# Performance work log

Hardware: AMD Instinct MI355X
Metric: run time of the kernel (lower is better)

The kernel has to match this reference:

```python
import jax, jax.numpy as jnp
import numpy as np

N, E = 50000, 800000
IN, HID, OUT, H = 128, 64, 64, 2
NC, EC = 5, 2  # node / edge num classes
NUM_ITER, GAMMA = 2, 1.0


def gat_conv(x, src, dst, eattr, W, att_s, att_d, We, att_e, b, n_nodes):
    """PyG GATConv with concat=False, edge_dim, add_self_loops(fill='mean')."""
    Hh, C = att_s.shape
    # self loops; loop edge_attr = per-dst-node mean of incident edge features
    ones_e = jnp.ones((src.shape[0],), x.dtype)
    deg = jax.ops.segment_sum(ones_e, dst, num_segments=n_nodes)
    loop_attr = jax.ops.segment_sum(eattr, dst, num_segments=n_nodes) / jnp.maximum(deg, 1.0)[:, None]
    loop = jnp.arange(n_nodes)
    src = jnp.concatenate([src, loop])
    dst = jnp.concatenate([dst, loop])
    eattr = jnp.concatenate([eattr, loop_attr], axis=0)
    h = (x @ W).reshape(n_nodes, Hh, C)            # [N,H,C]
    e = (eattr @ We).reshape(-1, Hh, C)            # [E',H,C]
    a_s = jnp.einsum('nhc,hc->nh', h, att_s)
    a_d = jnp.einsum('nhc,hc->nh', h, att_d)
    a_e = jnp.einsum('ehc,hc->eh', e, att_e)
    a = jax.nn.leaky_relu(a_s[src] + a_d[dst] + a_e, 0.2)  # [E',H]
    amax = jax.ops.segment_max(a, dst, num_segments=n_nodes)
    ea = jnp.exp(a - amax[dst])
    denom = jax.ops.segment_sum(ea, dst, num_segments=n_nodes)
    alpha = ea / (denom[dst] + 1e-16)
    out = jax.ops.segment_sum(alpha[:, :, None] * h[src], dst, num_segments=n_nodes)
    return out.mean(axis=1) + b                     # concat=False -> head mean


def factor_graph(node_logits, edge_logits, src, dst, node_fw, edge_fw):
    n = node_logits.shape[0]
    p_n = jax.nn.softmax(node_logits, axis=-1)
    p_e = jax.nn.softmax(edge_logits, axis=-1)
    ones_e = jnp.ones((src.shape[0],), node_logits.dtype)
    deg = jax.ops.segment_sum(ones_e, src, num_segments=n) + jax.ops.segment_sum(ones_e, dst, num_segments=n)
    avg_ef = edge_fw[1:, 1:].mean()
    avg_nf = node_fw[1:, 1:].mean()
    for _ in range(NUM_ITER):
        nab = 1.0 - p_n[:, 0]
        ena = jnp.maximum(nab[src], nab[dst])                       # [E]
        new_ab = p_e[:, 1:] * (1.0 + GAMMA * ena[:, None] * avg_ef)
        p_e = jnp.concatenate([p_e[:, :1], new_ab], axis=-1)
        p_e = p_e / p_e.sum(axis=-1, keepdims=True)
        eab = 1.0 - p_e[:, 0]
        s = jax.ops.segment_sum(eab, src, num_segments=n) + jax.ops.segment_sum(eab, dst, num_segments=n)
        mean = s / (deg + 1e-6)
        new_nab = p_n[:, 1:] * (1.0 + GAMMA * mean[:, None] * avg_nf)
        p_n = jnp.concatenate([p_n[:, :1], new_nab], axis=-1)
        p_n = p_n / p_n.sum(axis=-1, keepdims=True)
    return jnp.log(p_n + 1e-9), jnp.log(p_e + 1e-9)


def setup_inputs() -> dict:
    key = jax.random.key(0)
    ks = jax.random.split(key, 24)
    s = 0.1
    d = dict(
        x=jax.random.normal(ks[0], (N, IN), jnp.float32),
        edge_index=jax.random.randint(ks[1], (2, E), 0, N),
        edge_attr=jax.random.normal(ks[2], (E, 2), jnp.float32),
        W1=jax.random.normal(ks[3], (IN, H * HID), jnp.float32) * s,
        att_src1=jax.random.normal(ks[4], (H, HID), jnp.float32) * s,
        att_dst1=jax.random.normal(ks[5], (H, HID), jnp.float32) * s,
        We1=jax.random.normal(ks[6], (2, H * HID), jnp.float32) * s,
        att_e1=jax.random.normal(ks[7], (H, HID), jnp.float32) * s,
        b1=jnp.zeros((HID,), jnp.float32),
        W2=jax.random.normal(ks[8], (HID, H * OUT), jnp.float32) * s,
        att_src2=jax.random.normal(ks[9], (H, OUT), jnp.float32) * s,
        att_dst2=jax.random.normal(ks[10], (H, OUT), jnp.float32) * s,
        We2=jax.random.normal(ks[11], (2, H * OUT), jnp.float32) * s,
        att_e2=jax.random.normal(ks[12], (H, OUT), jnp.float32) * s,
        b2=jnp.zeros((OUT,), jnp.float32),
        Wn=jax.random.normal(ks[13], (OUT, NC), jnp.float32) * s,
        bn=jnp.zeros((NC,), jnp.float32),
        Wec=jax.random.normal(ks[14], (OUT, EC), jnp.float32) * s,
        bec=jnp.zeros((EC,), jnp.float32),
        node_fw=jnp.ones((NC, EC), jnp.float32),
        edge_fw=jnp.ones((EC, NC), jnp.float32),
    )
    return d


def reference(x, edge_index, edge_attr, W1, att_src1, att_dst1, We1, att_e1, b1,
              W2, att_src2, att_dst2, We2, att_e2, b2, Wn, bn, Wec, bec,
              node_fw, edge_fw):
    src, dst = edge_index[0], edge_index[1]
    h = gat_conv(x, src, dst, edge_attr, W1, att_src1, att_dst1, We1, att_e1, b1, N)
    h = jax.nn.relu(h)
    h = gat_conv(h, src, dst, edge_attr, W2, att_src2, att_dst2, We2, att_e2, b2, N)
    node_logits = h @ Wn + bn                       # [N,NC]
    edge_emb = (h[src] + h[dst]) * 0.5              # [E,OUT]
    edge_logits = edge_emb @ Wec + bec              # [E,EC]
    return factor_graph(node_logits, edge_logits, src, dst, node_fw, edge_fw)
```

## Files before the change

### kernel.cpp

```cpp
#include <hip/hip_runtime.h>
#include <math.h>


static inline int cdiv_i(long long a, long long b) { return (int)((a + b - 1) / b); }

#define BSH 8
#define CBK 8

typedef __attribute__((ext_vector_type(8))) short bf16x8s;
typedef __attribute__((ext_vector_type(4))) float f32x4;

__device__ __forceinline__ float fexp(float x) {
  return __builtin_amdgcn_exp2f(x * 1.44269504088896f);
}
__device__ __forceinline__ float flog(float x) {
  return __builtin_amdgcn_logf(x) * 0.693147180559945f;
}
__device__ __forceinline__ float frcp(float x) {
  return __builtin_amdgcn_rcpf(x);
}

__device__ __forceinline__ unsigned short bf16r(float x) {
  unsigned u = __float_as_uint(x);
  return (unsigned short)((u + 0x7fffu + ((u >> 16) & 1u)) >> 16);
}
__device__ __forceinline__ unsigned pack_bf2(float a, float b) {
  unsigned ua = __float_as_uint(a), ub = __float_as_uint(b);
  unsigned ra = (ua + 0x7fffu + ((ua >> 16) & 1u)) >> 16;
  unsigned rb = (ub + 0x7fffu + ((ub >> 16) & 1u)) & 0xffff0000u;
  return ra | rb;
}
__device__ __forceinline__ float bf_lo(unsigned v) { return __uint_as_float(v << 16); }
__device__ __forceinline__ float bf_hi(unsigned v) { return __uint_as_float(v & 0xffff0000u); }

__global__ __launch_bounds__(256)
void k_prep(const float* __restrict__ W1, const float* __restrict__ as1,
            const float* __restrict__ ad1, const float* __restrict__ atte1,
            const float* __restrict__ We1,
            const float* __restrict__ W2, const float* __restrict__ as2,
            const float* __restrict__ ad2, const float* __restrict__ atte2,
            const float* __restrict__ We2,
            const float* __restrict__ node_fw, const float* __restrict__ edge_fw,
            const float* __restrict__ bec, float* __restrict__ consts,
            unsigned short* __restrict__ wf1, unsigned short* __restrict__ wf2,
            int* __restrict__ cur_d, int* __restrict__ cur_s) {
  __shared__ float wext1[128 * 4], wext2[64 * 4];
  int t = threadIdx.x;
  cur_d[t] = 0; cur_s[t] = 0;
  if (t == 0) {
    for (int h = 0; h < 2; ++h)
      for (int k = 0; k < 2; ++k) {
        float s1 = 0.f, s2 = 0.f;
        for (int c = 0; c < 64; ++c) {
          s1 += We1[k * 128 + h * 64 + c] * atte1[h * 64 + c];
          s2 += We2[k * 128 + h * 64 + c] * atte2[h * 64 + c];
        }
        consts[h * 2 + k] = s1;
        consts[4 + h * 2 + k] = s2;
      }
    float ef = 0.f;
    for (int j = 1; j < 5; ++j) ef += edge_fw[5 + j];
    consts[8] = ef * 0.25f;
    float nf = 0.f;
    for (int i = 1; i < 5; ++i) nf += node_fw[i * 2 + 1];
    consts[9] = nf * 0.25f;
    consts[10] = bec[1] - bec[0];
  }
  for (int o = t; o < 128 * 4; o += 256) {
    int k = o >> 2, j = o & 3;
    const float* att = (j < 2 ? as1 : ad1) + (j & 1) * 64;
    const float* wr = W1 + k * 128 + (j & 1) * 64;
    float s = 0.f;
    for (int c = 0; c < 64; ++c) s += wr[c] * att[c];
    wext1[o] = s;
  }
  for (int o = t; o < 64 * 4; o += 256) {
    int k = o >> 2, j = o & 3;
    const float* att = (j < 2 ? as2 : ad2) + (j & 1) * 64;
    const float* wr = W2 + k * 128 + (j & 1) * 64;
    float s = 0.f;
    for (int c = 0; c < 64; ++c) s += wr[c] * att[c];
    wext2[o] = s;
  }
  __syncthreads();
  for (int o = t; o < 4 * 9 * 512; o += 256) {
    int kc = o / (9 * 512), rem = o % (9 * 512);
    int ct = rem / 512, li = rem % 512;
    int lane = li >> 3, j = li & 7;
    int k = kc * 32 + ((lane >> 4) << 3) + j, c = lane & 15;
    float v = (ct < 8) ? W1[k * 128 + ct * 16 + c] : (c < 4 ? wext1[k * 4 + c] : 0.f);
    wf1[o] = bf16r(v);
  }
  for (int o = t; o < 2 * 9 * 512; o += 256) {
    int kc = o / (9 * 512), rem = o % (9 * 512);
    int ct = rem / 512, li = rem % 512;
    int lane = li >> 3, j = li & 7;
    int k = kc * 32 + ((lane >> 4) << 3) + j, c = lane & 15;
    float v = (ct < 8) ? W2[k * 128 + ct * 16 + c] : (c < 4 ? wext2[k * 4 + c] : 0.f);
    wf2[o] = bf16r(v);
  }
}

__global__ void k_bkt_hist(const int* __restrict__ src, const int* __restrict__ dst,
                           int* __restrict__ hist_d, int* __restrict__ hist_s,
                           int nbkt, int E) {
  __shared__ int hd[256], hs[256];
  int t = threadIdx.x;
  hd[t] = 0; hs[t] = 0;
  __syncthreads();
  for (int e = blockIdx.x * blockDim.x + t; e < E; e += gridDim.x * blockDim.x) {
    atomicAdd(&hd[dst[e] >> BSH], 1);
    atomicAdd(&hs[src[e] >> BSH], 1);
  }
  __syncthreads();
  if (t < nbkt) {
    if (hd[t]) atomicAdd(&hist_d[t], hd[t]);
    if (hs[t]) atomicAdd(&hist_s[t], hs[t]);
  }
}

__global__ void k_bkt_scan(int* __restrict__ cur_d, int* __restrict__ base_d,
                           int* __restrict__ cur_s, int* __restrict__ base_s, int nbkt) {
  __shared__ int l[256];
  int t = threadIdx.x;
  int v = (t < nbkt) ? cur_d[t] : 0;
  l[t] = v; __syncthreads();
  for (int off = 1; off < 256; off <<= 1) {
    int x = (t >= off) ? l[t - off] : 0; __syncthreads();
    l[t] += x; __syncthreads();
  }
  int incl = l[t];
  if (t < nbkt) { base_d[t] = incl - v; cur_d[t] = incl - v; }
  if (t == nbkt - 1) base_d[nbkt] = incl;
  __syncthreads();
  v = (t < nbkt) ? cur_s[t] : 0;
  l[t] = v; __syncthreads();
  for (int off = 1; off < 256; off <<= 1) {
    int x = (t >= off) ? l[t - off] : 0; __syncthreads();
    l[t] += x; __syncthreads();
  }
  incl = l[t];
  if (t < nbkt) { base_s[t] = incl - v; cur_s[t] = incl - v; }
  if (t == nbkt - 1) base_s[nbkt] = incl;
}

__global__ __launch_bounds__(256)
void k_bkt_scatter(const int* __restrict__ src, const int* __restrict__ dst,
                   const float* __restrict__ eattr2,
                   int* __restrict__ cur_d, int* __restrict__ cur_s,
                   int4* __restrict__ stage_d, int2* __restrict__ stage_s,
                   int nbkt, int E) {
  __shared__ int cd[256], cs[256], bd[256], bs[256];
  int t = threadIdx.x;
  cd[t] = 0; cs[t] = 0;
  __syncthreads();
  int base = blockIdx.x * 256 * CBK;
  int s[CBK], d[CBK]; unsigned ep[CBK];
#pragma unroll
  for (int c = 0; c < CBK; ++c) {
    int e = base + c * 256 + t;
    if (e < E) {
      s[c] = src[e]; d[c] = dst[e];
      float2 ev = *(const float2*)&eattr2[2 * e];
      ep[c] = pack_bf2(ev.x, ev.y);
      atomicAdd(&cd[d[c] >> BSH], 1);
      atomicAdd(&cs[s[c] >> BSH], 1);
    } else s[c] = -1;
  }
  __syncthreads();
  if (t < nbkt) {
    bd[t] = cd[t] ? atomicAdd(&cur_d[t], cd[t]) : 0;
    bs[t] = cs[t] ? atomicAdd(&cur_s[t], cs[t]) : 0;
    cd[t] = 0; cs[t] = 0;
  }
  __syncthreads();
#pragma unroll
  for (int c = 0; c < CBK; ++c) {
    if (s[c] < 0) continue;
    int db = d[c] >> BSH, sb = s[c] >> BSH;
    int pos = bd[db] + atomicAdd(&cd[db], 1);
    stage_d[pos] = make_int4(s[c], d[c], (int)ep[c], 0);
    int pos2 = bs[sb] + atomicAdd(&cs[sb], 1);
    stage_s[pos2] = make_int2(s[c], d[c]);
  }
}

__global__ __launch_bounds__(256)
void k_bkt_sort(const int4* __restrict__ stage_d, const int* __restrict__ base_d,
                int* __restrict__ rowptr_d, int2* __restrict__ rec,
                const int2* __restrict__ stage_s, const int* __restrict__ base_s,
                int* __restrict__ rowptr_s, int* __restrict__ srcnbr,
                int N, int nbkt) {
  int t = threadIdx.x;
  __shared__ int cnt[256], cur[256], l[256];
  if ((int)blockIdx.x < nbkt) {
    int b = blockIdx.x;
    int nlo = b << BSH;
    int b0 = base_d[b], b1 = base_d[b + 1];
    cnt[t] = 0;
    __syncthreads();
    for (int j = b0 + t; j < b1; j += 256)
      atomicAdd(&cnt[stage_d[j].y - nlo], 1);
    __syncthreads();
    int v = cnt[t];
    l[t] = v; __syncthreads();
    for (int off = 1; off < 256; off <<= 1) {
      int x = (t >= off) ? l[t - off] : 0; __syncthreads();
      l[t] += x; __syncthreads();
    }
    int excl = l[t] - v;
    if (nlo + t < N) rowptr_d[nlo + t] = b0 + excl;
    cur[t] = excl;
    __syncthreads();
    for (int j = b0 + t; j < b1; j += 256) {
      int4 r = stage_d[j];
      int pos = b0 + atomicAdd(&cur[r.y - nlo], 1);
      rec[pos] = make_int2(r.x, r.z);
    }
  } else {
    int b = blockIdx.x - nbkt;
    int nlo = b << BSH;
    int b0 = base_s[b], b1 = base_s[b + 1];
    cnt[t] = 0;
    __syncthreads();
    for (int j = b0 + t; j < b1; j += 256)
      atomicAdd(&cnt[stage_s[j].x - nlo], 1);
    __syncthreads();
    int v = cnt[t];
    l[t] = v; __syncthreads();
    for (int off = 1; off < 256; off <<= 1) {
      int x = (t >= off) ? l[t - off] : 0; __syncthreads();
      l[t] += x; __syncthreads();
    }
    int excl = l[t] - v;
    if (nlo + t < N) rowptr_s[nlo + t] = b0 + excl;
    cur[t] = excl;
    __syncthreads();
    for (int j = b0 + t; j < b1; j += 256) {
      int2 r = stage_s[j];
      int pos = b0 + atomicAdd(&cur[r.x - nlo], 1);
      srcnbr[pos] = r.y;
    }
  }
}

template<int K>
__global__ __launch_bounds__(256)
void k_gemm_att_mfma(const float* __restrict__ A, const unsigned short* __restrict__ Wf,
                     unsigned* __restrict__ h16, float* __restrict__ asd, int N) {
  int wv = threadIdx.x >> 6, lane = threadIdx.x & 63;
  int r0 = blockIdx.x * 64 + wv * 16;
  int arow = r0 + (lane & 15);
  int kbase = (lane >> 4) * 8;
  f32x4 acc[9];
#pragma unroll
  for (int ct = 0; ct < 9; ++ct) acc[ct] = (f32x4){0.f, 0.f, 0.f, 0.f};

#pragma unroll
  for (int kc = 0; kc < K; kc += 32) {
    float4 v0 = make_float4(0.f, 0.f, 0.f, 0.f);
    float4 v1 = make_float4(0.f, 0.f, 0.f, 0.f);
    if (arow < N) {
      const float* ap = A + (long long)arow * K + kc + kbase;
      v0 = *(const float4*)ap;
      v1 = *(const float4*)(ap + 4);
    }
    bf16x8s a;
    a[0] = (short)bf16r(v0.x); a[1] = (short)bf16r(v0.y);
    a[2] = (short)bf16r(v0.z); a[3] = (short)bf16r(v0.w);
    a[4] = (short)bf16r(v1.x); a[5] = (short)bf16r(v1.y);
    a[6] = (short)bf16r(v1.z); a[7] = (short)bf16r(v1.w);
    const unsigned short* wp = Wf + (size_t)(kc >> 5) * 9 * 512 + lane * 8;
#pragma unroll
    for (int ct = 0; ct < 9; ++ct) {
      bf16x8s b = *(const bf16x8s*)(wp + ct * 512);
      acc[ct] = __builtin_amdgcn_mfma_f32_16x16x32_bf16(a, b, acc[ct], 0, 0, 0);
    }
  }
  int c = lane & 15;
  int orow = r0 + (lane >> 4) * 4;
#pragma unroll
  for (int r = 0; r < 4; ++r) {
    int gr = orow + r;
    if (gr >= N) continue;
#pragma unroll
    for (int ct = 0; ct < 4; ++ct)
      h16[((long long)gr << 6) | (ct * 16 + c)] = pack_bf2(acc[ct][r], acc[ct + 4][r]);
    if (c < 4) asd[gr * 4 + c] = acc[8][r];
  }
}

template<bool RELU, bool HEAD>
__global__ __launch_bounds__(256)
void k_gat_pull(const int* __restrict__ rowptr, const int2* __restrict__ rec,
                const float* __restrict__ asd, const unsigned* __restrict__ h16,
                const float* __restrict__ we, const float* __restrict__ bias,
                const float* __restrict__ Wn, const float* __restrict__ bn,
                const float* __restrict__ Wec,
                float* __restrict__ out, float* __restrict__ p_n,
                int2* __restrict__ fgn8, int N, int E) {
  __shared__ int2 ed[4][64];
  int wv = threadIdx.x >> 6, lane = threadIdx.x & 63;
  int g = lane >> 4;
  int tl = lane & 15;
  int d = blockIdx.x * 16 + wv * 4 + g;
  if (d >= N) return;
  int r0 = rowptr[d];
  int r1 = (d + 1 < N) ? rowptr[d + 1] : E;
  int deg = r1 - r0;
  float4 Ad = *(const float4*)&asd[4 * d];
  float w0 = we[0], w1 = we[1], w2 = we[2], w3 = we[3];
  float den0 = 0.f, den1 = 0.f, se0 = 0.f, se1 = 0.f;
  float accA[4] = {0.f, 0.f, 0.f, 0.f}, accB[4] = {0.f, 0.f, 0.f, 0.f};
  int2* edg = &ed[wv][g << 4];
  for (int cb = 0; cb < deg; cb += 16) {
    int j = cb + tl;
    int s = 0; unsigned eapk = 0;
    if (j < deg) {
      int2 rc = rec[r0 + j];
      s = rc.x;
      unsigned ep = (unsigned)rc.y;
      float e0 = bf_lo(ep), e1 = bf_hi(ep);
      float4 As = *(const float4*)&asd[4 * s];
      float x0 = As.x + Ad.z + e0 * w0 + e1 * w1;
      float x1 = As.y + Ad.w + e0 * w2 + e1 * w3;
      x0 = x0 >= 0.f ? x0 : 0.2f * x0;
      x1 = x1 >= 0.f ? x1 : 0.2f * x1;
      float ea0 = fexp(x0), ea1 = fexp(x1);
      eapk = pack_bf2(ea0, ea1);
      den0 += ea0; den1 += ea1; se0 += e0; se1 += e1;
    }
    edg[tl] = make_int2(s, (int)eapk);
    int m = min(16, deg - cb);
    int j2 = 0;
    for (; j2 + 2 <= m; j2 += 2) {
      int2 va = edg[j2];
      int2 vb = edg[j2 + 1];
      uint4 qa = *(const uint4*)&h16[((long long)va.x << 6) | (tl << 2)];
      uint4 qb = *(const uint4*)&h16[((long long)vb.x << 6) | (tl << 2)];
      float a0 = bf_lo((unsigned)va.y), a1 = bf_hi((unsigned)va.y);
      float b0 = bf_lo((unsigned)vb.y), b1 = bf_hi((unsigned)vb.y);
      accA[0] += a0 * bf_lo(qa.x); accB[0] += a1 * bf_hi(qa.x);
      accA[1] += a0 * bf_lo(qa.y); accB[1] += a1 * bf_hi(qa.y);
      accA[2] += a0 * bf_lo(qa.z); accB[2] += a1 * bf_hi(qa.z);
      accA[3] += a0 * bf_lo(qa.w); accB[3] += a1 * bf_hi(qa.w);
      accA[0] += b0 * bf_lo(qb.x); accB[0] += b1 * bf_hi(qb.x);
      accA[1] += b0 * bf_lo(qb.y); accB[1] += b1 * bf_hi(qb.y);
      accA[2] += b0 * bf_lo(qb.z); accB[2] += b1 * bf_hi(qb.z);
      accA[3] += b0 * bf_lo(qb.w); accB[3] += b1 * bf_hi(qb.w);
    }
    if (j2 < m) {
      int2 va = edg[j2];
      uint4 qa = *(const uint4*)&h16[((long long)va.x << 6) | (tl << 2)];
      float a0 = bf_lo((unsigned)va.y), a1 = bf_hi((unsigned)va.y);
      accA[0] += a0 * bf_lo(qa.x); accB[0] += a1 * bf_hi(qa.x);
      accA[1] += a0 * bf_lo(qa.y); accB[1] += a1 * bf_hi(qa.y);
      accA[2] += a0 * bf_lo(qa.z); accB[2] += a1 * bf_hi(qa.z);
      accA[3] += a0 * bf_lo(qa.w); accB[3] += a1 * bf_hi(qa.w);
    }
  }
  for (int off = 8; off; off >>= 1) {
    den0 += __shfl_xor(den0, off); den1 += __shfl_xor(den1, off);
    se0  += __shfl_xor(se0, off);  se1  += __shfl_xor(se1, off);
  }
  float id = frcp(fmaxf((float)deg, 1.0f));
  float le0 = se0 * id, le1 = se1 * id;
  float x0 = Ad.x + Ad.z + le0 * w0 + le1 * w1;
  float x1 = Ad.y + Ad.w + le0 * w2 + le1 * w3;
  x0 = x0 >= 0.f ? x0 : 0.2f * x0;
  x1 = x1 >= 0.f ? x1 : 0.2f * x1;
  float eas0 = fexp(x0), eas1 = fexp(x1);
  den0 += eas0; den1 += eas1;
  uint4 qd = *(const uint4*)&h16[((long long)d << 6) | (tl << 2)];
  accA[0] += eas0 * bf_lo(qd.x); accB[0] += eas1 * bf_hi(qd.x);
  accA[1] += eas0 * bf_lo(qd.y); accB[1] += eas1 * bf_hi(qd.y);
  accA[2] += eas0 * bf_lo(qd.z); accB[2] += eas1 * bf_hi(qd.z);
  accA[3] += eas0 * bf_lo(qd.w); accB[3] += eas1 * bf_hi(qd.w);
  float rcp0 = frcp(den0 + 1e-16f), rcp1 = frcp(den1 + 1e-16f);
  float4 bs = *(const float4*)&bias[tl << 2];
  float v0 = 0.5f * (accA[0] * rcp0 + accB[0] * rcp1) + bs.x;
  float v1 = 0.5f * (accA[1] * rcp0 + accB[1] * rcp1) + bs.y;
  float v2 = 0.5f * (accA[2] * rcp0 + accB[2] * rcp1) + bs.z;
  float v3 = 0.5f * (accA[3] * rcp0 + accB[3] * rcp1) + bs.w;
  if (HEAD) {
    int c0 = tl << 2;
    float pv[7];
#pragma unroll
    for (int j = 0; j < 5; ++j)
      pv[j] = v0 * Wn[c0 * 5 + j] + v1 * Wn[(c0 + 1) * 5 + j]
            + v2 * Wn[(c0 + 2) * 5 + j] + v3 * Wn[(c0 + 3) * 5 + j];
    pv[5] = v0 * Wec[c0 * 2] + v1 * Wec[(c0 + 1) * 2]
          + v2 * Wec[(c0 + 2) * 2] + v3 * Wec[(c0 + 3) * 2];
    pv[6] = v0 * Wec[c0 * 2 + 1] + v1 * Wec[(c0 + 1) * 2 + 1]
          + v2 * Wec[(c0 + 2) * 2 + 1] + v3 * Wec[(c0 + 3) * 2 + 1];
    for (int off = 8; off; off >>= 1) {
#pragma unroll
      for (int j = 0; j < 7; ++j) pv[j] += __shfl_xor(pv[j], off);
    }
    if (tl == 0) {
      float l[5]; float m = -1e30f;
#pragma unroll
      for (int j = 0; j < 5; ++j) { l[j] = pv[j] + bn[j]; m = fmaxf(m, l[j]); }
      float ssum = 0.f;
#pragma unroll
      for (int j = 0; j < 5; ++j) { l[j] = fexp(l[j] - m); ssum += l[j]; }
      float inv = frcp(ssum);
#pragma unroll
      for (int j = 0; j < 5; ++j) p_n[5 * d + j] = l[j] * inv;
      float nab0 = (ssum - l[0]) * inv;
      fgn8[d] = make_int2(__float_as_int(pv[6] - pv[5]), (int)pack_bf2(nab0, 0.f));
    }
  } else {
    if (RELU) {
      v0 = fmaxf(v0, 0.f); v1 = fmaxf(v1, 0.f);
      v2 = fmaxf(v2, 0.f); v3 = fmaxf(v3, 0.f);
    }
    *(float4*)&out[(long long)d * 64 + (tl << 2)] = make_float4(v0, v1, v2, v3);
  }
}

__device__ __forceinline__ float fg_eab(float t, float c) {
  return c * frcp(c + fexp(-t));
}

__global__ void k_fg_pull1(const int* __restrict__ rowptr_d, const int2* __restrict__ rec,
                           const int* __restrict__ rowptr_s, const int* __restrict__ srcnbr,
                           float* __restrict__ p_n, int2* __restrict__ fgn8,
                           const float* __restrict__ consts, int N, int E) {
  int gid = blockIdx.x * blockDim.x + threadIdx.x;
  int n = gid >> 2, q = gid & 3;
  if (n >= N) return;
  int2 F = fgn8[n];
  float qv = __uint_as_float((unsigned)F.x);
  float nab0 = bf_lo((unsigned)F.y);
  float avg_ef = consts[8], avg_nf = consts[9], dbec = consts[10];
  int rd0 = rowptr_d[n], rd1 = (n + 1 < N) ? rowptr_d[n + 1] : E;
  int rs0 = rowptr_s[n], rs1 = (n + 1 < N) ? rowptr_s[n + 1] : E;
  float s_eab = 0.f;
  for (int j = rd0 + q; j < rd1; j += 4) {
    int2 Fo = fgn8[rec[j].x];
    float t = 0.5f * (qv + __uint_as_float((unsigned)Fo.x)) + dbec;
    float c = 1.0f + fmaxf(nab0, bf_lo((unsigned)Fo.y)) * avg_ef;
    s_eab += fg_eab(t, c);
  }
  for (int j = rs0 + q; j < rs1; j += 4) {
    int2 Fo = fgn8[srcnbr[j]];
    float t = 0.5f * (qv + __uint_as_float((unsigned)Fo.x)) + dbec;
    float c = 1.0f + fmaxf(nab0, bf_lo((unsigned)Fo.y)) * avg_ef;
    s_eab += fg_eab(t, c);
  }
  s_eab += __shfl_xor(s_eab, 1);
  s_eab += __shfl_xor(s_eab, 2);
  if (q) return;
  float deg = (float)((rd1 - rd0) + (rs1 - rs0));
  float mean = s_eab * frcp(deg + 1e-6f);
  float f = 1.0f + mean * avg_nf;
  float p0 = p_n[5 * n], p1 = p_n[5 * n + 1], p2 = p_n[5 * n + 2],
        p3 = p_n[5 * n + 3], p4 = p_n[5 * n + 4];
  float rest = (p1 + p2 + p3 + p4) * f;
  float inv = frcp(p0 + rest);
  p_n[5 * n]     = p0 * inv;
  p_n[5 * n + 1] = p1 * f * inv;
  p_n[5 * n + 2] = p2 * f * inv;
  p_n[5 * n + 3] = p3 * f * inv;
  p_n[5 * n + 4] = p4 * f * inv;
  fgn8[n].y = (int)pack_bf2(nab0, rest * inv);
}

__global__ void k_fg_final(const int* __restrict__ rowptr_d, const int2* __restrict__ rec,
                           const int* __restrict__ rowptr_s, const int* __restrict__ srcnbr,
                           const float* __restrict__ p_n, const int2* __restrict__ fgn8,
                           const float* __restrict__ consts,
                           const int* __restrict__ src, const int* __restrict__ dst,
                           float* __restrict__ out_n, float* __restrict__ out_e,
                           int N, int E, int nodeBlocks) {
  float avg_ef = consts[8], dbec = consts[10];
  if ((int)blockIdx.x < nodeBlocks) {
    int gid = blockIdx.x * blockDim.x + threadIdx.x;
    int n = gid >> 2, q = gid & 3;
    if (n >= N) return;
    float avg_nf = consts[9];
    int2 F = fgn8[n];
    float qv = __uint_as_float((unsigned)F.x);
    float nab0 = bf_lo((unsigned)F.y), nab1 = bf_hi((unsigned)F.y);
    int rd0 = rowptr_d[n], rd1 = (n + 1 < N) ? rowptr_d[n + 1] : E;
    int rs0 = rowptr_s[n], rs1 = (n + 1 < N) ? rowptr_s[n + 1] : E;
    float s_eab = 0.f;
    for (int j = rd0 + q; j < rd1; j += 4) {
      int2 Fo = fgn8[rec[j].x];
      float t = 0.5f * (qv + __uint_as_float((unsigned)Fo.x)) + dbec;
      float c = (1.0f + fmaxf(nab0, bf_lo((unsigned)Fo.y)) * avg_ef)
              * (1.0f + fmaxf(nab1, bf_hi((unsigned)Fo.y)) * avg_ef);
      s_eab += fg_eab(t, c);
    }
    for (int j = rs0 + q; j < rs1; j += 4) {
      int2 Fo = fgn8[srcnbr[j]];
      float t = 0.5f * (qv + __uint_as_float((unsigned)Fo.x)) + dbec;
      float c = (1.0f + fmaxf(nab0, bf_lo((unsigned)Fo.y)) * avg_ef)
              * (1.0f + fmaxf(nab1, bf_hi((unsigned)Fo.y)) * avg_ef);
      s_eab += fg_eab(t, c);
    }
    s_eab += __shfl_xor(s_eab, 1);
    s_eab += __shfl_xor(s_eab, 2);
    if (q) return;
    float deg = (float)((rd1 - rd0) + (rs1 - rs0));
    float mean = s_eab * frcp(deg + 1e-6f);
    float f = 1.0f + mean * avg_nf;
    float p0 = p_n[5 * n], p1 = p_n[5 * n + 1], p2 = p_n[5 * n + 2],
          p3 = p_n[5 * n + 3], p4 = p_n[5 * n + 4];
    float rest = (p1 + p2 + p3 + p4) * f;
    float inv = frcp(p0 + rest);
    out_n[5 * n]     = flog(p0 * inv + 1e-9f);
    out_n[5 * n + 1] = flog(p1 * f * inv + 1e-9f);
    out_n[5 * n + 2] = flog(p2 * f * inv + 1e-9f);
    out_n[5 * n + 3] = flog(p3 * f * inv + 1e-9f);
    out_n[5 * n + 4] = flog(p4 * f * inv + 1e-9f);
  } else {
    int e = (blockIdx.x - nodeBlocks) * blockDim.x + threadIdx.x;
    if (e >= E) return;
    int2 Fs = fgn8[src[e]];
    int2 Fd = fgn8[dst[e]];
    float t = 0.5f * (__uint_as_float((unsigned)Fs.x) + __uint_as_float((unsigned)Fd.x)) + dbec;
    float c = (1.0f + fmaxf(bf_lo((unsigned)Fs.y), bf_lo((unsigned)Fd.y)) * avg_ef)
            * (1.0f + fmaxf(bf_hi((unsigned)Fs.y), bf_hi((unsigned)Fd.y)) * avg_ef);
    float ei = fexp(-t);
    float r = frcp(c + ei);
    float pe1 = c * r, pe0 = ei * r;
    *(float2*)&out_e[2 * e] = make_float2(flog(pe0 + 1e-9f), flog(pe1 + 1e-9f));
  }
}

extern "C" void kernel_launch(void* const* d_in, const int* in_sizes, int n_in,
                              void* d_out, int out_size, void* d_ws, size_t ws_size,
                              hipStream_t stream) {
  const float* x      = (const float*)d_in[0];
  const int*   ei     = (const int*)d_in[1];
  const float* eattr  = (const float*)d_in[2];
  const float* W1     = (const float*)d_in[3];
  const float* atts1  = (const float*)d_in[4];
  const float* attd1  = (const float*)d_in[5];
  const float* We1    = (const float*)d_in[6];
  const float* atte1  = (const float*)d_in[7];
  const float* b1     = (const float*)d_in[8];
  const float* W2     = (const float*)d_in[9];
  const float* atts2  = (const float*)d_in[10];
  const float* attd2  = (const float*)d_in[11];
  const float* We2    = (const float*)d_in[12];
  const float* atte2  = (const float*)d_in[13];
  const float* b2     = (const float*)d_in[14];
  const float* Wn     = (const float*)d_in[15];
  const float* bn     = (const float*)d_in[16];
  const float* Wec    = (const float*)d_in[17];
  const float* bec    = (const float*)d_in[18];
  const float* nodefw = (const float*)d_in[19];
  const float* edgefw = (const float*)d_in[20];

  const int N = in_sizes[0] / 128;
  const int E = in_sizes[1] / 2;
  const int* src = ei;
  const int* dst = ei + E;
  const int nbkt = (N + 255) >> BSH;

  float* out_n = (float*)d_out;
  float* out_e = out_n + (long long)N * 5;

  size_t off = 0;
  float* base = (float*)d_ws;
  auto carve = [&](size_t nelem) { float* p = base + off; off += (nelem + 3) & ~(size_t)3; return p; };
  unsigned* h16      = (unsigned*)carve((size_t)N * 64);
  float*    x2       = carve((size_t)N * 64);
  float*    asd      = carve((size_t)N * 4);
  int2*     rec      = (int2*)carve((size_t)E * 2);
  int*      srcnbr   = (int*)carve((size_t)E);
  int*      rowptr_d = (int*)carve((size_t)N);
  int*      rowptr_s = (int*)carve((size_t)N);
  int*      bktcur_d = (int*)carve(256);
  int*      bktcur_s = (int*)carve(256);
  int*      bktbas_d = (int*)carve(260);
  int*      bktbas_s = (int*)carve(260);
  float*    p_n      = carve((size_t)N * 5);
  int2*     fgn8     = (int2*)carve((size_t)N * 2);
  float*    consts   = carve(16);
  unsigned short* wf1 = (unsigned short*)carve(9216);
  unsigned short* wf2 = (unsigned short*)carve(4608);
  if (off * sizeof(float) > ws_size) return;

  int4* stage_d = (int4*)h16;
  int2* stage_s = (int2*)x2;

  const int B = 256;
  const int gE  = cdiv_i(E, B);
  const int gN4 = cdiv_i((long long)N * 4, B);

  k_prep<<<1, 256, 0, stream>>>(W1, atts1, attd1, atte1, We1,
                                W2, atts2, attd2, atte2, We2,
                                nodefw, edgefw, bec, consts, wf1, wf2,
                                bktcur_d, bktcur_s);
  k_bkt_hist<<<256, 256, 0, stream>>>(src, dst, bktcur_d, bktcur_s, nbkt, E);
  k_bkt_scan<<<1, 256, 0, stream>>>(bktcur_d, bktbas_d, bktcur_s, bktbas_s, nbkt);
  k_bkt_scatter<<<cdiv_i(E, 256 * CBK), 256, 0, stream>>>(src, dst, eattr, bktcur_d, bktcur_s,
                                                          stage_d, stage_s, nbkt, E);
  k_bkt_sort<<<2 * nbkt, 256, 0, stream>>>(stage_d, bktbas_d, rowptr_d, rec,
                                           stage_s, bktbas_s, rowptr_s, srcnbr, N, nbkt);

  k_gemm_att_mfma<128><<<cdiv_i(N, 64), 256, 0, stream>>>(x, wf1, h16, asd, N);
  k_gat_pull<true, false><<<cdiv_i(N, 16), 256, 0, stream>>>(
      rowptr_d, rec, asd, h16, consts, b1,
      nullptr, nullptr, nullptr, x2, nullptr, nullptr, N, E);

  k_gemm_att_mfma<64><<<cdiv_i(N, 64), 256, 0, stream>>>(x2, wf2, h16, asd, N);
  k_gat_pull<false, true><<<cdiv_i(N, 16), 256, 0, stream>>>(
      rowptr_d, rec, asd, h16, consts + 4, b2,
      Wn, bn, Wec, nullptr, p_n, fgn8, N, E);

  k_fg_pull1<<<gN4, B, 0, stream>>>(rowptr_d, rec, rowptr_s, srcnbr,
                                    p_n, fgn8, consts, N, E);
  k_fg_final<<<gN4 + gE, B, 0, stream>>>(rowptr_d, rec, rowptr_s, srcnbr,
                                         p_n, fgn8, consts, src, dst,
                                         out_n, out_e, N, E, gN4);
}
```

Measured before the change: 219.5 us.

## Unroll GAT gather loop, add compact dst-neighbor array, batch edge outputs

The bucket sort now also writes a compact int array of source neighbors per destination row. The factor-graph pulls read this array instead of the wider int2 rec records, halving the bytes they load. The GAT pull's neighbor-aggregation loop is unrolled to eight and four gathers at a time so more independent loads are in flight. The edge-output tail of the final kernel now handles two edges per thread. The cost is extra workspace, an extra store stream during sorting, and higher register pressure in the unrolled loop.

```diff
diff --git a/kernel.cpp b/kernel.cpp
--- a/kernel.cpp
+++ b/kernel.cpp
@@ -188,6 +188,7 @@
 __global__ __launch_bounds__(256)
 void k_bkt_sort(const int4* __restrict__ stage_d, const int* __restrict__ base_d,
                 int* __restrict__ rowptr_d, int2* __restrict__ rec,
+                int* __restrict__ dstnbr,
                 const int2* __restrict__ stage_s, const int* __restrict__ base_s,
                 int* __restrict__ rowptr_s, int* __restrict__ srcnbr,
                 int N, int nbkt) {
@@ -216,6 +217,7 @@
       int4 r = stage_d[j];
       int pos = b0 + atomicAdd(&cur[r.y - nlo], 1);
       rec[pos] = make_int2(r.x, r.z);
+      dstnbr[pos] = r.x;
     }
   } else {
     int b = blockIdx.x - nbkt;
@@ -333,23 +335,40 @@
     edg[tl] = make_int2(s, (int)eapk);
     int m = min(16, deg - cb);
     int j2 = 0;
-    for (; j2 + 2 <= m; j2 += 2) {
-      int2 va = edg[j2];
-      int2 vb = edg[j2 + 1];
-      uint4 qa = *(const uint4*)&h16[((long long)va.x << 6) | (tl << 2)];
-      uint4 qb = *(const uint4*)&h16[((long long)vb.x << 6) | (tl << 2)];
-      float a0 = bf_lo((unsigned)va.y), a1 = bf_hi((unsigned)va.y);
-      float b0 = bf_lo((unsigned)vb.y), b1 = bf_hi((unsigned)vb.y);
-      accA[0] += a0 * bf_lo(qa.x); accB[0] += a1 * bf_hi(qa.x);
-      accA[1] += a0 * bf_lo(qa.y); accB[1] += a1 * bf_hi(qa.y);
-      accA[2] += a0 * bf_lo(qa.z); accB[2] += a1 * bf_hi(qa.z);
-      accA[3] += a0 * bf_lo(qa.w); accB[3] += a1 * bf_hi(qa.w);
-      accA[0] += b0 * bf_lo(qb.x); accB[0] += b1 * bf_hi(qb.x);
-      accA[1] += b0 * bf_lo(qb.y); accB[1] += b1 * bf_hi(qb.y);
-      accA[2] += b0 * bf_lo(qb.z); accB[2] += b1 * bf_hi(qb.z);
-      accA[3] += b0 * bf_lo(qb.w); accB[3] += b1 * bf_hi(qb.w);
-    }
-    if (j2 < m) {
+    for (; j2 + 8 <= m; j2 += 8) {
+      int2 v[8]; uint4 q[8];
+#pragma unroll
+      for (int u = 0; u < 8; ++u) v[u] = edg[j2 + u];
+#pragma unroll
+      for (int u = 0; u < 8; ++u)
+        q[u] = *(const uint4*)&h16[((long long)v[u].x << 6) | (tl << 2)];
+#pragma unroll
+      for (int u = 0; u < 8; ++u) {
+        float a0 = bf_lo((unsigned)v[u].y), a1 = bf_hi((unsigned)v[u].y);
+        accA[0] += a0 * bf_lo(q[u].x); accB[0] += a1 * bf_hi(q[u].x);
+        accA[1] += a0 * bf_lo(q[u].y); accB[1] += a1 * bf_hi(q[u].y);
+        accA[2] += a0 * bf_lo(q[u].z); accB[2] += a1 * bf_hi(q[u].z);
+        accA[3] += a0 * bf_lo(q[u].w); accB[3] += a1 * bf_hi(q[u].w);
+      }
+    }
+    if (j2 + 4 <= m) {
+      int2 v[4]; uint4 q[4];
+#pragma unroll
+      for (int u = 0; u < 4; ++u) v[u] = edg[j2 + u];
+#pragma unroll
+      for (int u = 0; u < 4; ++u)
+        q[u] = *(const uint4*)&h16[((long long)v[u].x << 6) | (tl << 2)];
+#pragma unroll
+      for (int u = 0; u < 4; ++u) {
+        float a0 = bf_lo((unsigned)v[u].y), a1 = bf_hi((unsigned)v[u].y);
+        accA[0] += a0 * bf_lo(q[u].x); accB[0] += a1 * bf_hi(q[u].x);
+        accA[1] += a0 * bf_lo(q[u].y); accB[1] += a1 * bf_hi(q[u].y);
+        accA[2] += a0 * bf_lo(q[u].z); accB[2] += a1 * bf_hi(q[u].z);
+        accA[3] += a0 * bf_lo(q[u].w); accB[3] += a1 * bf_hi(q[u].w);
+      }
+      j2 += 4;
+    }
+    for (; j2 < m; ++j2) {
       int2 va = edg[j2];
       uint4 qa = *(const uint4*)&h16[((long long)va.x << 6) | (tl << 2)];
       float a0 = bf_lo((unsigned)va.y), a1 = bf_hi((unsigned)va.y);
@@ -423,7 +442,7 @@
   return c * frcp(c + fexp(-t));
 }
 
-__global__ void k_fg_pull1(const int* __restrict__ rowptr_d, const int2* __restrict__ rec,
+__global__ void k_fg_pull1(const int* __restrict__ rowptr_d, const int* __restrict__ dstnbr,
                            const int* __restrict__ rowptr_s, const int* __restrict__ srcnbr,
                            float* __restrict__ p_n, int2* __restrict__ fgn8,
                            const float* __restrict__ consts, int N, int E) {
@@ -438,7 +457,7 @@
   int rs0 = rowptr_s[n], rs1 = (n + 1 < N) ? rowptr_s[n + 1] : E;
   float s_eab = 0.f;
   for (int j = rd0 + q; j < rd1; j += 4) {
-    int2 Fo = fgn8[rec[j].x];
+    int2 Fo = fgn8[dstnbr[j]];
     float t = 0.5f * (qv + __uint_as_float((unsigned)Fo.x)) + dbec;
     float c = 1.0f + fmaxf(nab0, bf_lo((unsigned)Fo.y)) * avg_ef;
     s_eab += fg_eab(t, c);
@@ -467,7 +486,7 @@
   fgn8[n].y = (int)pack_bf2(nab0, rest * inv);
 }
 
-__global__ void k_fg_final(const int* __restrict__ rowptr_d, const int2* __restrict__ rec,
+__global__ void k_fg_final(const int* __restrict__ rowptr_d, const int* __restrict__ dstnbr,
                            const int* __restrict__ rowptr_s, const int* __restrict__ srcnbr,
                            const float* __restrict__ p_n, const int2* __restrict__ fgn8,
                            const float* __restrict__ consts,
@@ -487,7 +506,7 @@
     int rs0 = rowptr_s[n], rs1 = (n + 1 < N) ? rowptr_s[n + 1] : E;
     float s_eab = 0.f;
     for (int j = rd0 + q; j < rd1; j += 4) {
-      int2 Fo = fgn8[rec[j].x];
+      int2 Fo = fgn8[dstnbr[j]];
       float t = 0.5f * (qv + __uint_as_float((unsigned)Fo.x)) + dbec;
       float c = (1.0f + fmaxf(nab0, bf_lo((unsigned)Fo.y)) * avg_ef)
               * (1.0f + fmaxf(nab1, bf_hi((unsigned)Fo.y)) * avg_ef);
@@ -516,17 +535,30 @@
     out_n[5 * n + 3] = flog(p3 * f * inv + 1e-9f);
     out_n[5 * n + 4] = flog(p4 * f * inv + 1e-9f);
   } else {
-    int e = (blockIdx.x - nodeBlocks) * blockDim.x + threadIdx.x;
-    if (e >= E) return;
-    int2 Fs = fgn8[src[e]];
-    int2 Fd = fgn8[dst[e]];
-    float t = 0.5f * (__uint_as_float((unsigned)Fs.x) + __uint_as_float((unsigned)Fd.x)) + dbec;
-    float c = (1.0f + fmaxf(bf_lo((unsigned)Fs.y), bf_lo((unsigned)Fd.y)) * avg_ef)
-            * (1.0f + fmaxf(bf_hi((unsigned)Fs.y), bf_hi((unsigned)Fd.y)) * avg_ef);
-    float ei = fexp(-t);
-    float r = frcp(c + ei);
-    float pe1 = c * r, pe0 = ei * r;
-    *(float2*)&out_e[2 * e] = make_float2(flog(pe0 + 1e-9f), flog(pe1 + 1e-9f));
+    int e0 = ((blockIdx.x - nodeBlocks) * blockDim.x + threadIdx.x) * 2;
+    if (e0 >= E) return;
+    int ne = min(2, E - e0);
+    int sv[2], dv[2];
+#pragma unroll
+    for (int u = 0; u < 2; ++u) {
+      sv[u] = (u < ne) ? src[e0 + u] : 0;
+      dv[u] = (u < ne) ? dst[e0 + u] : 0;
+    }
+    int2 Fs[2], Fd[2];
+#pragma unroll
+    for (int u = 0; u < 2; ++u) { Fs[u] = fgn8[sv[u]]; Fd[u] = fgn8[dv[u]]; }
+#pragma unroll
+    for (int u = 0; u < 2; ++u) {
+      if (u >= ne) break;
+      float t = 0.5f * (__uint_as_float((unsigned)Fs[u].x) +
+                        __uint_as_float((unsigned)Fd[u].x)) + dbec;
+      float c = (1.0f + fmaxf(bf_lo((unsigned)Fs[u].y), bf_lo((unsigned)Fd[u].y)) * avg_ef)
+              * (1.0f + fmaxf(bf_hi((unsigned)Fs[u].y), bf_hi((unsigned)Fd[u].y)) * avg_ef);
+      float ei = fexp(-t);
+      float r = frcp(c + ei);
+      float pe1 = c * r, pe0 = ei * r;
+      *(float2*)&out_e[2 * (e0 + u)] = make_float2(flog(pe0 + 1e-9f), flog(pe1 + 1e-9f));
+    }
   }
 }
 
@@ -572,6 +604,7 @@
   float*    asd      = carve((size_t)N * 4);
   int2*     rec      = (int2*)carve((size_t)E * 2);
   int*      srcnbr   = (int*)carve((size_t)E);
+  int*      dstnbr   = (int*)carve((size_t)E);
   int*      rowptr_d = (int*)carve((size_t)N);
   int*      rowptr_s = (int*)carve((size_t)N);
   int*      bktcur_d = (int*)carve(256);
@@ -589,7 +622,7 @@
   int2* stage_s = (int2*)x2;
 
   const int B = 256;
-  const int gE  = cdiv_i(E, B);
+  const int gE2 = cdiv_i((long long)E, B * 2);
   const int gN4 = cdiv_i((long long)N * 4, B);
 
   k_prep<<<1, 256, 0, stream>>>(W1, atts1, attd1, atte1, We1,
@@ -600,7 +633,7 @@
   k_bkt_scan<<<1, 256, 0, stream>>>(bktcur_d, bktbas_d, bktcur_s, bktbas_s, nbkt);
   k_bkt_scatter<<<cdiv_i(E, 256 * CBK), 256, 0, stream>>>(src, dst, eattr, bktcur_d, bktcur_s,
                                                           stage_d, stage_s, nbkt, E);
-  k_bkt_sort<<<2 * nbkt, 256, 0, stream>>>(stage_d, bktbas_d, rowptr_d, rec,
+  k_bkt_sort<<<2 * nbkt, 256, 0, stream>>>(stage_d, bktbas_d, rowptr_d, rec, dstnbr,
                                            stage_s, bktbas_s, rowptr_s, srcnbr, N, nbkt);
 
   k_gemm_att_mfma<128><<<cdiv_i(N, 64), 256, 0, stream>>>(x, wf1, h16, asd, N);
@@ -613,9 +646,9 @@
       rowptr_d, rec, asd, h16, consts + 4, b2,
       Wn, bn, Wec, nullptr, p_n, fgn8, N, E);
 
-  k_fg_pull1<<<gN4, B, 0, stream>>>(rowptr_d, rec, rowptr_s, srcnbr,
+  k_fg_pull1<<<gN4, B, 0, stream>>>(rowptr_d, dstnbr, rowptr_s, srcnbr,
                                     p_n, fgn8, consts, N, E);
-  k_fg_final<<<gN4 + gE, B, 0, stream>>>(rowptr_d, rec, rowptr_s, srcnbr,
-                                         p_n, fgn8, consts, src, dst,
-                                         out_n, out_e, N, E, gN4);
-}
+  k_fg_final<<<gN4 + gE2, B, 0, stream>>>(rowptr_d, dstnbr, rowptr_s, srcnbr,
+                                          p_n, fgn8, consts, src, dst,
+                                          out_n, out_e, N, E, gN4);
+}
```

After: 225.7 us. 1.03x slower.
